# Kernel optimization log

Hardware: AMD Instinct MI355X
Metric: run time of the kernel (lower is better)

## Reference

```python
import jax, jax.numpy as jnp
import numpy as np

B, T, C = 4, 2048, 1024
NH = 16
HS = C // NH


def setup_inputs() -> dict:
    key = jax.random.key(0)
    ks = jax.random.split(key, 11)
    s = 1.0 / np.sqrt(C)
    inp = {
        "query": jax.random.normal(ks[0], (B, T, C), jnp.float32),
        "key": jax.random.normal(ks[1], (B, T, C), jnp.float32),
        "value": jax.random.normal(ks[2], (B, T, C), jnp.float32),
        # causal mask: 1.0 where attention is disallowed (j > i)
        "mask": jnp.triu(jnp.ones((T, T), jnp.float32), k=1)[None, None, :, :],
        "Wq": jax.random.normal(ks[3], (C, C), jnp.float32) * s,
        "bq": jnp.zeros((C,), jnp.float32),
        "Wk": jax.random.normal(ks[4], (C, C), jnp.float32) * s,
        "bk": jnp.zeros((C,), jnp.float32),
        "Wv": jax.random.normal(ks[5], (C, C), jnp.float32) * s,
        "bv": jnp.zeros((C,), jnp.float32),
        "Wo": jax.random.normal(ks[6], (C, C), jnp.float32) * s,
        "bo": jnp.zeros((C,), jnp.float32),
    }
    return inp


def _split_heads(x):  # [B,T,C] -> [B,NH,T,HS]
    Bq, Tq, Cq = x.shape
    return x.reshape(Bq, Tq, NH, Cq // NH).transpose(0, 2, 1, 3)


def reference(query, key, value, mask, Wq, bq, Wk, bk, Wv, bv, Wo, bo):
    q = _split_heads(query @ Wq + bq)   # [B,NH,T,HS]
    k = _split_heads(key @ Wk + bk)
    v = _split_heads(value @ Wv + bv)
    scores = jnp.einsum("bhqd,bhkd->bhqk", q, k) / jnp.sqrt(jnp.asarray(HS, q.dtype))
    scores = scores + mask * (-1e9)
    attn = jax.nn.softmax(scores, axis=-1)
    out = jnp.einsum("bhqk,bhkd->bhqd", attn, v)     # [B,NH,T,HS]
    out = out.transpose(0, 2, 1, 3).reshape(query.shape[0], query.shape[1], -1)
    return out @ Wo + bo
```

## Files before the change

kernel.cpp:

```cpp
#include <hip/hip_runtime.h>
#include <hip/hip_bf16.h>
#include <stdint.h>

#define B_ 4
#define T_ 2048
#define C_ 1024
#define NH_ 16
#define HS_ 64

using bf16 = __hip_bfloat16;
typedef __bf16 bf16x8 __attribute__((ext_vector_type(8)));
typedef float f32x4 __attribute__((ext_vector_type(4)));
typedef short short8 __attribute__((ext_vector_type(8)));

__device__ __forceinline__ f32x4 mfma16(bf16x8 a, bf16x8 b, f32x4 c) {
    return __builtin_amdgcn_mfma_f32_16x16x32_bf16(a, b, c, 0, 0, 0);
}

__device__ __forceinline__ float fexp2(float x) {
    return __builtin_amdgcn_exp2f(x);
}

__device__ __forceinline__ short bf16bits(float f) {
    __bf16 b = (__bf16)f;
    return *reinterpret_cast<short*>(&b);
}

__device__ __forceinline__ void gload16(const void* g, void* l) {
    __builtin_amdgcn_global_load_lds(
        (const __attribute__((address_space(1))) void*)g,
        (__attribute__((address_space(3))) void*)l, 16, 0, 0);
}

__device__ __forceinline__ short8 load8(const bf16* p) { return *(const short8*)p; }
__device__ __forceinline__ short8 load8(const float* p) {
    float4 f0 = *(const float4*)p;
    float4 f1 = *(const float4*)(p + 4);
    short8 r;
    r[0] = bf16bits(f0.x); r[1] = bf16bits(f0.y); r[2] = bf16bits(f0.z); r[3] = bf16bits(f0.w);
    r[4] = bf16bits(f1.x); r[5] = bf16bits(f1.y); r[6] = bf16bits(f1.z); r[7] = bf16bits(f1.w);
    return r;
}

__device__ __forceinline__ void storev(bf16* p, float v) { *p = __float2bfloat16(v); }
__device__ __forceinline__ void storev(float* p, float v) { *p = v; }

__device__ __forceinline__ int lds_rd(int row, int lg) {
    return row * 64 + (((lg - (row >> 1)) & 3) << 4);
}

__global__ __launch_bounds__(256) void prep_kernel(
    const float* __restrict__ Xq, const float* __restrict__ Xk,
    const float* __restrict__ Xv,
    bf16* __restrict__ XbA, bf16* __restrict__ XbB, bf16* __restrict__ XbC,
    const float* __restrict__ Wq, const float* __restrict__ Wk,
    const float* __restrict__ Wv, const float* __restrict__ Wo,
    bf16* __restrict__ WqT, bf16* __restrict__ WkT,
    bf16* __restrict__ WvT, bf16* __restrict__ WoT)
{
    const int bid = blockIdx.x;
    if (bid < 12288) {
        const int z = bid >> 12;
        const int chunk = bid & 4095;
        const float* s = (z == 0) ? Xq : (z == 1) ? Xk : Xv;
        bf16* d       = (z == 0) ? XbA : (z == 1) ? XbB : XbC;
        const size_t i = ((size_t)chunk * 256 + threadIdx.x) * 8;
        *(short8*)(d + i) = load8(s + i);
        return;
    }
    const int tt = bid - 12288;
    const int z  = tt >> 8;
    const int by = ((tt & 255) >> 4) * 64;
    const int bx = (tt & 15) * 64;
    const float* in = (z == 0) ? Wq : (z == 1) ? Wk : (z == 2) ? Wv : Wo;
    bf16* out      = (z == 0) ? WqT : (z == 1) ? WkT : (z == 2) ? WvT : WoT;

    __shared__ short tile[64][80];
    const int t = threadIdx.x;
    const int r = t >> 3, c8 = (t & 7) * 8;
    *(short8*)&tile[r][c8]      = load8(in + (size_t)(by + r) * 1024 + bx + c8);
    *(short8*)&tile[r + 32][c8] = load8(in + (size_t)(by + r + 32) * 1024 + bx + c8);
    __syncthreads();
    short8 v0, v1;
    #pragma unroll
    for (int i = 0; i < 8; ++i) {
        v0[i] = tile[c8 + i][r];
        v1[i] = tile[c8 + i][r + 32];
    }
    *(short8*)(out + (size_t)(bx + r) * 1024 + by + c8)      = v0;
    *(short8*)(out + (size_t)(bx + r + 32) * 1024 + by + c8) = v1;
}

template <typename OutT>
__device__ __forceinline__ void gemm_body(
    const bf16* __restrict__ A, const bf16* __restrict__ BT,
    const float* __restrict__ bias, OutT* __restrict__ out,
    int M, int N, int K, int mode, float oscale)
{
    __shared__ __align__(16) short As[2][128 * 32];
    __shared__ __align__(16) short Bs[2][128 * 32];
    const int tid = threadIdx.x;
    const int lane = tid & 63;
    const int w = tid >> 6;
    const int wm = w >> 1, wn = w & 1;
    const int lg = lane >> 4, lr = lane & 15;
    const int bm = blockIdx.x * 128;
    const int bn = blockIdx.y * 128;

    const int grow = w * 16 + (lane >> 2);
    const int gch  = ((lane & 3) + (grow >> 1)) & 3;
    const bf16* gB0 = BT + (size_t)(bn + grow) * K + gch * 8;
    const bf16* gA0 = A  + (size_t)(bm + grow) * K + gch * 8;
    const int lofs = w * 1024;

    f32x4 acc[4][4] = {};

    gload16(gB0,                  (char*)Bs[0] + lofs);
    gload16(gB0 + (size_t)64 * K, (char*)Bs[0] + lofs + 4096);
    gload16(gA0,                  (char*)As[0] + lofs);
    gload16(gA0 + (size_t)64 * K, (char*)As[0] + lofs + 4096);

    int c = 0;
    for (int k0 = 0; k0 < K; k0 += 32) {
        __syncthreads();
        if (k0 + 32 < K) {
            gload16(gB0 + k0 + 32,                  (char*)Bs[c ^ 1] + lofs);
            gload16(gB0 + (size_t)64 * K + k0 + 32, (char*)Bs[c ^ 1] + lofs + 4096);
            gload16(gA0 + k0 + 32,                  (char*)As[c ^ 1] + lofs);
            gload16(gA0 + (size_t)64 * K + k0 + 32, (char*)As[c ^ 1] + lofs + 4096);
        }
        bf16x8 af[4], bfv[4];
        #pragma unroll
        for (int i = 0; i < 4; ++i) {
            af[i]  = *(const bf16x8*)((char*)As[c] + lds_rd(wm * 64 + i * 16 + lr, lg));
            bfv[i] = *(const bf16x8*)((char*)Bs[c] + lds_rd(wn * 64 + i * 16 + lr, lg));
        }
        #pragma unroll
        for (int mi = 0; mi < 4; ++mi)
            #pragma unroll
            for (int nj = 0; nj < 4; ++nj)
                acc[mi][nj] = mfma16(af[mi], bfv[nj], acc[mi][nj]);
        c ^= 1;
    }

    #pragma unroll
    for (int mi = 0; mi < 4; ++mi) {
        #pragma unroll
        for (int nj = 0; nj < 4; ++nj) {
            const int n = bn + wn * 64 + nj * 16 + lr;
            const float bv = bias[n];
            #pragma unroll
            for (int r = 0; r < 4; ++r) {
                const int m = bm + wm * 64 + mi * 16 + lg * 4 + r;
                const float val = (acc[mi][nj][r] + bv) * oscale;
                size_t idx;
                if (mode == 1) {
                    idx = (size_t)((m >> 11) * NH_ + (n >> 6)) * (T_ * HS_)
                        + (size_t)(m & (T_ - 1)) * HS_ + (n & (HS_ - 1));
                } else if (mode == 2) {
                    idx = (size_t)((m >> 11) * NH_ + (n >> 6)) * (T_ * HS_)
                        + (size_t)(n & (HS_ - 1)) * T_ + (m & (T_ - 1));
                } else {
                    idx = (size_t)m * N + n;
                }
                storev(out + idx, val);
            }
        }
    }
}

__global__ __launch_bounds__(256) void gemm_qkv_kernel(
    const bf16* __restrict__ XbA, const bf16* __restrict__ XbB,
    const bf16* __restrict__ XbC,
    const bf16* __restrict__ WqT, const bf16* __restrict__ WkT,
    const bf16* __restrict__ WvT,
    const float* __restrict__ bq, const float* __restrict__ bk,
    const float* __restrict__ bv,
    bf16* __restrict__ Qh, bf16* __restrict__ Kh, bf16* __restrict__ VtG)
{
    const int z = blockIdx.z;
    const bf16* A   = (z == 0) ? XbA : (z == 1) ? XbB : XbC;
    const bf16* BT  = (z == 0) ? WqT : (z == 1) ? WkT : WvT;
    const float* bs = (z == 0) ? bq : (z == 1) ? bk : bv;
    bf16* out       = (z == 0) ? Qh : (z == 1) ? Kh : VtG;
    const float sc  = (z == 0) ? 0.18033688f : 1.0f;
    gemm_body<bf16>(A, BT, bs, out, 8192, 1024, 1024, (z == 2) ? 2 : 1, sc);
}

__global__ __launch_bounds__(256) void gemm_out_kernel(
    const bf16* __restrict__ A, const bf16* __restrict__ BT,
    const float* __restrict__ bias, float* __restrict__ out)
{
    gemm_body<float>(A, BT, bias, out, 8192, 1024, 1024, 0, 1.0f);
}

__global__ __launch_bounds__(512, 4) void attn_kernel(
    const bf16* __restrict__ Qh, const bf16* __restrict__ Kh,
    const bf16* __restrict__ Vt, bf16* __restrict__ Ob)
{
    __shared__ __align__(16) char Ks[2][8192];
    __shared__ __align__(16) char Vs[2][8192];
    __shared__ __align__(16) char Ps[8][2][2048];

    const int tid  = threadIdx.x;
    const int lane = tid & 63;
    const int w    = tid >> 6;
    const int lg = lane >> 4, lr = lane & 15;
    const int bh = blockIdx.x;
    const int bq = blockIdx.y;
    const size_t hb = (size_t)bh * (T_ * HS_);

    const int s_lo = bq * 8 + w;
    const int s_hi = 127 - s_lo;
    const int qbase[2] = { s_lo * 16, s_hi * 16 };
    const int last_t[2] = { s_lo >> 2, s_hi >> 2 };
    const int nt = 32 - 2 * bq;

    const int swzp = (lr & 7) << 4;

    const int strow = tid >> 3;
    const int stch  = tid & 7;
    const int stdst = strow * 128 + ((stch ^ (strow & 7)) << 4);
    const bf16* gK = Kh + hb + (size_t)strow * HS_ + stch * 8;
    const bf16* gV = Vt + hb + (size_t)strow * T_  + stch * 8;

    bf16x8 qf[2][2];
    #pragma unroll
    for (int qs = 0; qs < 2; ++qs)
        #pragma unroll
        for (int kfi = 0; kfi < 2; ++kfi)
            qf[qs][kfi] = *(const bf16x8*)(Qh + hb + (size_t)(qbase[qs] + lr) * HS_ + kfi * 32 + lg * 8);

    f32x4 accO[2][4] = {};
    float l_s[2] = {0.f, 0.f};
    char* pwq[2] = {&Ps[w][0][0], &Ps[w][1][0]};

    uint4 kst = *(const uint4*)(gK);
    uint4 vst = *(const uint4*)(gV);
    *(uint4*)(&Ks[0][stdst]) = kst;
    *(uint4*)(&Vs[0][stdst]) = vst;
    __syncthreads();

    int c = 0;
    for (int t = 0; t < nt; ++t) {
        if (t + 1 < nt) {
            kst = *(const uint4*)(gK + (size_t)(t + 1) * 64 * HS_);
            vst = *(const uint4*)(gV + (t + 1) * 64);
        }
        const int j0 = t * 64;
        const char* Kc = &Ks[c][0];
        const char* Vc = &Vs[c][0];
        const bool act[2] = { t <= last_t[0], t <= last_t[1] };

        bf16x8 kfr[4][2];
        #pragma unroll
        for (int s = 0; s < 4; ++s)
            #pragma unroll
            for (int kfi = 0; kfi < 2; ++kfi)
                kfr[s][kfi] = *(const bf16x8*)(Kc + (s * 16 + lr) * 128 + (((kfi * 4 + lg) ^ (lr & 7)) << 4));

        #pragma unroll
        for (int qs = 0; qs < 2; ++qs) {
            if (!act[qs]) continue;
            f32x4 st[4];
            #pragma unroll
            for (int s = 0; s < 4; ++s) {
                f32x4 a = {};
                #pragma unroll
                for (int kfi = 0; kfi < 2; ++kfi)
                    a = mfma16(kfr[s][kfi], qf[qs][kfi], a);
                st[s] = a;
            }
            float p[4][4];
            float rs = 0.f;
            #pragma unroll
            for (int s = 0; s < 4; ++s)
                #pragma unroll
                for (int r = 0; r < 4; ++r) {
                    p[s][r] = fexp2(st[s][r]);
                    rs += p[s][r];
                }
            if (t == last_t[qs]) {
                const int q = qbase[qs] + lr;
                rs = 0.f;
                #pragma unroll
                for (int s = 0; s < 4; ++s)
                    #pragma unroll
                    for (int r = 0; r < 4; ++r) {
                        if (j0 + s * 16 + 4 * lg + r > q) p[s][r] = 0.f;
                        rs += p[s][r];
                    }
            }
            l_s[qs] += rs;
            #pragma unroll
            for (int s = 0; s < 4; ++s) {
                uint2 pk;
                pk.x = (uint16_t)bf16bits(p[s][0]) | ((uint32_t)(uint16_t)bf16bits(p[s][1]) << 16);
                pk.y = (uint16_t)bf16bits(p[s][2]) | ((uint32_t)(uint16_t)bf16bits(p[s][3]) << 16);
                *(uint2*)(pwq[qs] + ((lr * 128 + s * 32 + lg * 8) ^ swzp)) = pk;
            }
        }
        __builtin_amdgcn_wave_barrier();

        bf16x8 vfr[4][2];
        #pragma unroll
        for (int d = 0; d < 4; ++d)
            #pragma unroll
            for (int kfi = 0; kfi < 2; ++kfi)
                vfr[d][kfi] = *(const bf16x8*)(Vc + (d * 16 + lr) * 128 + (((kfi * 4 + lg) ^ (lr & 7)) << 4));

        #pragma unroll
        for (int qs = 0; qs < 2; ++qs) {
            if (!act[qs]) continue;
            bf16x8 aP[2];
            #pragma unroll
            for (int kfi = 0; kfi < 2; ++kfi)
                aP[kfi] = *(const bf16x8*)(pwq[qs] + ((lr * 128 + kfi * 64 + lg * 16) ^ swzp));
            #pragma unroll
            for (int d = 0; d < 4; ++d)
                #pragma unroll
                for (int kfi = 0; kfi < 2; ++kfi)
                    accO[qs][d] = mfma16(aP[kfi], vfr[d][kfi], accO[qs][d]);
        }

        if (t + 1 < nt) {
            *(uint4*)(&Ks[c ^ 1][stdst]) = kst;
            *(uint4*)(&Vs[c ^ 1][stdst]) = vst;
        }
        __syncthreads();
        c ^= 1;
    }

    const int b = bh >> 4, h = bh & 15;
    #pragma unroll
    for (int qs = 0; qs < 2; ++qs) {
        float lsv[4];
        #pragma unroll
        for (int r = 0; r < 4; ++r) {
            float acc = 0.f;
            #pragma unroll
            for (int g = 0; g < 4; ++g)
                acc += __shfl(l_s[qs], 4 * lg + r + 16 * g);
            lsv[r] = acc;
        }
        #pragma unroll
        for (int d = 0; d < 4; ++d)
            #pragma unroll
            for (int r = 0; r < 4; ++r) {
                const int q = qbase[qs] + 4 * lg + r;
                const float o = accO[qs][d][r] / lsv[r];
                Ob[(((size_t)b * T_ + q) * NH_ + h) * HS_ + d * 16 + lr] = __float2bfloat16(o);
            }
    }
}

extern "C" void kernel_launch(void* const* d_in, const int* in_sizes, int n_in,
                              void* d_out, int out_size, void* d_ws, size_t ws_size,
                              hipStream_t stream)
{
    (void)in_sizes; (void)n_in; (void)out_size; (void)ws_size;
    const float* Xq = (const float*)d_in[0];
    const float* Xk = (const float*)d_in[1];
    const float* Xv = (const float*)d_in[2];
    const float* Wq = (const float*)d_in[4];
    const float* bq = (const float*)d_in[5];
    const float* Wk = (const float*)d_in[6];
    const float* bk = (const float*)d_in[7];
    const float* Wv = (const float*)d_in[8];
    const float* bv = (const float*)d_in[9];
    const float* Wo = (const float*)d_in[10];
    const float* bo = (const float*)d_in[11];

    char* ws = (char*)d_ws;
    bf16* WqT = (bf16*)(ws + ((size_t)0  << 20));
    bf16* WkT = (bf16*)(ws + ((size_t)2  << 20));
    bf16* WvT = (bf16*)(ws + ((size_t)4  << 20));
    bf16* WoT = (bf16*)(ws + ((size_t)6  << 20));
    bf16* XbA = (bf16*)(ws + ((size_t)8  << 20));
    bf16* XbB = (bf16*)(ws + ((size_t)24 << 20));
    bf16* Qh  = (bf16*)(ws + ((size_t)40 << 20));
    bf16* Kh  = (bf16*)(ws + ((size_t)56 << 20));
    bf16* VtG = (bf16*)(ws + ((size_t)72 << 20));
    bf16* XbC = (bf16*)d_out;
    bf16* Ob  = XbA;

    dim3 blk(256);
    prep_kernel<<<dim3(13312), blk, 0, stream>>>(
        Xq, Xk, Xv, XbA, XbB, XbC,
        Wq, Wk, Wv, Wo, WqT, WkT, WvT, WoT);

    gemm_qkv_kernel<<<dim3(64, 8, 3), blk, 0, stream>>>(
        XbA, XbB, XbC, WqT, WkT, WvT, bq, bk, bv, Qh, Kh, VtG);

    attn_kernel<<<dim3(64, 8), dim3(512), 0, stream>>>(Qh, Kh, VtG, Ob);

    gemm_out_kernel<<<dim3(64, 8), blk, 0, stream>>>(Ob, WoT, bo, (float*)d_out);
}
```

Before: 193.8 us.

## Triple-buffer GEMM LDS tiles with partial vmcnt waits

```diff
diff --git a/kernel.cpp b/kernel.cpp
--- a/kernel.cpp
+++ b/kernel.cpp
@@ -97,8 +97,8 @@
     const float* __restrict__ bias, OutT* __restrict__ out,
     int M, int N, int K, int mode, float oscale)
 {
-    __shared__ __align__(16) short As[2][128 * 32];
-    __shared__ __align__(16) short Bs[2][128 * 32];
+    __shared__ __align__(16) short As[3][128 * 32];
+    __shared__ __align__(16) short Bs[3][128 * 32];
     const int tid = threadIdx.x;
     const int lane = tid & 63;
     const int w = tid >> 6;
@@ -115,32 +115,42 @@
 
     f32x4 acc[4][4] = {};
 
-    gload16(gB0,                  (char*)Bs[0] + lofs);
-    gload16(gB0 + (size_t)64 * K, (char*)Bs[0] + lofs + 4096);
-    gload16(gA0,                  (char*)As[0] + lofs);
-    gload16(gA0 + (size_t)64 * K, (char*)As[0] + lofs + 4096);
-
-    int c = 0;
-    for (int k0 = 0; k0 < K; k0 += 32) {
-        __syncthreads();
-        if (k0 + 32 < K) {
-            gload16(gB0 + k0 + 32,                  (char*)Bs[c ^ 1] + lofs);
-            gload16(gB0 + (size_t)64 * K + k0 + 32, (char*)Bs[c ^ 1] + lofs + 4096);
-            gload16(gA0 + k0 + 32,                  (char*)As[c ^ 1] + lofs);
-            gload16(gA0 + (size_t)64 * K + k0 + 32, (char*)As[c ^ 1] + lofs + 4096);
-        }
+    #pragma unroll
+    for (int p = 0; p < 2; ++p) {
+        gload16(gB0 + p * 32,                  (char*)Bs[p] + lofs);
+        gload16(gB0 + (size_t)64 * K + p * 32, (char*)Bs[p] + lofs + 4096);
+        gload16(gA0 + p * 32,                  (char*)As[p] + lofs);
+        gload16(gA0 + (size_t)64 * K + p * 32, (char*)As[p] + lofs + 4096);
+    }
+
+    const int NT = K >> 5;
+    int c = 0, pp = 2;
+    for (int t = 0; t < NT; ++t) {
+        if (t == NT - 1) asm volatile("s_waitcnt vmcnt(0)" ::: "memory");
+        else             asm volatile("s_waitcnt vmcnt(4)" ::: "memory");
+        __builtin_amdgcn_s_barrier();
+        if (t + 2 < NT) {
+            const int k2 = (t + 2) << 5;
+            gload16(gB0 + k2,                  (char*)Bs[pp] + lofs);
+            gload16(gB0 + (size_t)64 * K + k2, (char*)Bs[pp] + lofs + 4096);
+            gload16(gA0 + k2,                  (char*)As[pp] + lofs);
+            gload16(gA0 + (size_t)64 * K + k2, (char*)As[pp] + lofs + 4096);
+        }
+        const char* Ac = (const char*)As[c];
+        const char* Bc = (const char*)Bs[c];
         bf16x8 af[4], bfv[4];
         #pragma unroll
         for (int i = 0; i < 4; ++i) {
-            af[i]  = *(const bf16x8*)((char*)As[c] + lds_rd(wm * 64 + i * 16 + lr, lg));
-            bfv[i] = *(const bf16x8*)((char*)Bs[c] + lds_rd(wn * 64 + i * 16 + lr, lg));
+            af[i]  = *(const bf16x8*)(Ac + lds_rd(wm * 64 + i * 16 + lr, lg));
+            bfv[i] = *(const bf16x8*)(Bc + lds_rd(wn * 64 + i * 16 + lr, lg));
         }
         #pragma unroll
         for (int mi = 0; mi < 4; ++mi)
             #pragma unroll
             for (int nj = 0; nj < 4; ++nj)
                 acc[mi][nj] = mfma16(af[mi], bfv[nj], acc[mi][nj]);
-        c ^= 1;
+        c = (c == 2) ? 0 : c + 1;
+        pp = (pp == 2) ? 0 : pp + 1;
     }
 
     #pragma unroll
```

New measurement: 218.9 us. +13.0%, slower.
